# Kernel tuning notes

Measured on AMD Instinct MI355X. Metric: run time of the kernel, lower is better.

## Reference

```python
import jax, jax.numpy as jnp
import numpy as np

WS = (2, 6, 12)          # window (Wz, Wh, Ww)
SHIFT = (1, 3, 6)        # Wz//2, Wh//2, Ww//2
NUM_HEADS = 8
DIM = 256
HIDDEN = 1024            # mlp_ratio * dim
TYPE_OF_WINDOWS = 64     # (Z//Wz)*(H//Wh)
EPS = 1e-5


def _build_position_index(ws):
    Wz, Wh, Ww = ws
    zi = np.arange(Wz); zj = -np.arange(Wz) * Wz
    hi = np.arange(Wh); hj = -np.arange(Wh) * Wh
    w = np.arange(Ww)
    gzi, ghi, gw = np.meshgrid(zi, hi, w, indexing='ij')
    gzj, ghj, _ = np.meshgrid(zj, hj, w, indexing='ij')
    fi = np.stack([gzi.ravel(), ghi.ravel(), gw.ravel()])
    fj = np.stack([gzj.ravel(), ghj.ravel(), gw.ravel()])
    coords = fi[:, :, None] - fj[:, None, :]
    coords[2] += Ww - 1
    coords[1] *= 2 * Ww - 1
    coords[0] *= (2 * Ww - 1) * Wh * Wh
    return coords.sum(0).reshape(-1)  # (N*N,) int


def _window_partition(x, ws):
    # (B, Z, H, W, C) -> (B*n_windows, Wz*Wh*Ww, C)
    B, Z, H, W, C = x.shape
    Wz, Wh, Ww = ws
    x = x.reshape(B, Z // Wz, Wz, H // Wh, Wh, W // Ww, Ww, C)
    x = x.transpose(0, 1, 3, 5, 2, 4, 6, 7)
    return x.reshape(-1, Wz * Wh * Ww, C)


def _window_reverse(win, ws, B, Z, H, W):
    Wz, Wh, Ww = ws
    x = win.reshape(B, Z // Wz, H // Wh, W // Ww, Wz, Wh, Ww, -1)
    x = x.transpose(0, 1, 4, 2, 5, 3, 6, 7)
    return x.reshape(B, Z, H, W, -1)


def _build_shift_mask(Z, H, W, ws, shift):
    Wz, Wh, Ww = ws
    sz, sh, sw = shift
    img = np.zeros((1, Z, H, W, 1), dtype=np.float32)
    z_slices = (slice(0, -Wz), slice(-Wz, -sz), slice(-sz, None))
    h_slices = (slice(0, -Wh), slice(-Wh, -sh), slice(-sh, None))
    w_slices = (slice(0, -Ww), slice(-Ww, -sw), slice(-sw, None))
    cnt = 0
    for zs in z_slices:
        for hs in h_slices:
            for wsl in w_slices:
                img[:, zs, hs, wsl, :] = cnt
                cnt += 1
    m = _window_partition(img, ws)[..., 0]             # (n_w, N)
    am = m[:, None, :] - m[:, :, None]                 # (n_w, N, N)
    am = np.where(am != 0, -100.0, 0.0).astype(np.float32)
    return am[:, None]                                 # (n_w, 1, N, N)


def _ln(x, g, b):
    mu = x.mean(-1, keepdims=True)
    var = ((x - mu) ** 2).mean(-1, keepdims=True)
    return (x - mu) * jax.lax.rsqrt(var + EPS) * g + b


def setup_inputs() -> dict:
    key = jax.random.key(0)
    ks = jax.random.split(key, 16)
    B, Z, H, W, C = 1, 8, 96, 192, DIM
    n_unique = (2 * WS[2] - 1) * WS[1] * WS[1] * WS[0] * WS[0]  # 3312
    s = 0.02
    return {
        'x': jax.random.normal(ks[0], (B, Z * H * W, C), jnp.float32),
        'g1': jnp.ones((C,), jnp.float32),
        'beta1': jnp.zeros((C,), jnp.float32),
        'wqkv': jax.random.normal(ks[1], (3 * C, C), jnp.float32) * s,
        'bqkv': jnp.zeros((3 * C,), jnp.float32),
        'bias_table': jax.random.normal(ks[2], (n_unique, TYPE_OF_WINDOWS, NUM_HEADS), jnp.float32) * s,
        'wproj': jax.random.normal(ks[3], (C, C), jnp.float32) * s,
        'bproj': jnp.zeros((C,), jnp.float32),
        'g2': jnp.ones((C,), jnp.float32),
        'beta2': jnp.zeros((C,), jnp.float32),
        'w1': jax.random.normal(ks[4], (HIDDEN, C), jnp.float32) * s,
        'b1': jnp.zeros((HIDDEN,), jnp.float32),
        'w2': jax.random.normal(ks[5], (C, HIDDEN), jnp.float32) * s,
        'b2': jnp.zeros((C,), jnp.float32),
        'Z': Z, 'H': H, 'W': W, 'window_type_index': 0,
    }


def reference(x, g1, beta1, wqkv, bqkv, bias_table, wproj, bproj, g2, beta2,
              w1, b1, w2, b2, Z, H, W, window_type_index):
    B, L, C = x.shape
    hd = C // NUM_HEADS
    scale = hd ** (-0.5)
    N = WS[0] * WS[1] * WS[2]

    xs = _ln(x, g1, beta1).reshape(B, Z, H, W, C)
    # shift
    xs = jnp.roll(xs, (-SHIFT[0], -SHIFT[1], -SHIFT[2]), axis=(1, 2, 3))
    mask = jnp.asarray(_build_shift_mask(Z, H, W, WS, SHIFT))  # (n_w,1,N,N)

    win = _window_partition(xs, WS)                    # (Bw, N, C)
    Bw = win.shape[0]
    qkv = (win @ wqkv.T + bqkv).reshape(Bw, N, 3, NUM_HEADS, hd).transpose(2, 0, 3, 1, 4)
    q, k, v = qkv[0], qkv[1], qkv[2]                   # (Bw, h, N, hd)

    attn = jnp.einsum('bhnd,bhmd->bhnm', q * scale, k)
    pos_index = _build_position_index(WS)              # (N*N,)
    bias = bias_table[pos_index, window_type_index]    # (N*N, heads)
    bias = bias.reshape(N, N, NUM_HEADS).transpose(2, 0, 1)[None]
    attn = attn + bias

    n_w = mask.shape[0]
    attn = attn.reshape(B, n_w, NUM_HEADS, N, N) + mask[None]
    attn = jax.nn.softmax(attn, axis=-1).reshape(Bw, NUM_HEADS, N, N)

    out = jnp.einsum('bhnm,bhmd->bhnd', attn, v).transpose(0, 2, 1, 3).reshape(Bw, N, C)
    out = out @ wproj.T + bproj

    xr = _window_reverse(out, WS, B, Z, H, W)
    xr = jnp.roll(xr, SHIFT, axis=(1, 2, 3)).reshape(B, Z * H * W, C)

    x = x + xr
    h = _ln(x, g2, beta2)
    h = jax.nn.gelu(h @ w1.T + b1, approximate=False)
    h = h @ w2.T + b2
    return x + h
```

## Files before the change

### kernel.cpp

```cpp
#include <hip/hip_runtime.h>
#include <hip/hip_bf16.h>
#include <math.h>

#define L_TOK   147456
#define CDIM    256
#define C3      768
#define HID     1024
#define NWIN    1024
#define NTOK    144
#define NHEADS  8
#define HD      32
#define SCALE   0.1767766952966369f

typedef __attribute__((ext_vector_type(8))) short bfrag;
typedef __attribute__((ext_vector_type(4))) float f32x4;

__device__ __forceinline__ ushort f2bf(float f) {
    __hip_bfloat16 h = __float2bfloat16(f);
    return *reinterpret_cast<ushort*>(&h);
}
__device__ __forceinline__ float bf2f(ushort u) {
    __hip_bfloat16 h = *reinterpret_cast<__hip_bfloat16*>(&u);
    return __bfloat162float(h);
}

__device__ __forceinline__ void gld16(const ushort* g, ushort* l) {
    __builtin_amdgcn_global_load_lds(
        (const __attribute__((address_space(1))) void*)g,
        (__attribute__((address_space(3))) void*)l, 16, 0, 0);
}

__device__ __forceinline__ int shift_src(int gt) {
    const int win = gt / NTOK;
    const int nt  = gt - win * NTOK;
    const int wz = win >> 8, wh = (win >> 4) & 15, ww = win & 15;
    const int lz = nt / 72;
    const int t2 = nt - lz * 72;
    const int lh = t2 / 12, lw = t2 - lh * 12;
    const int z = (wz * 2 + lz + 1) & 7;
    int h = wh * 6 + lh + 3;  if (h >= 96)  h -= 96;
    int w = ww * 12 + lw + 6; if (w >= 192) w -= 192;
    return (z * 96 + h) * 192 + w;
}

__global__ __launch_bounds__(256) void ln1_kernel(const float* __restrict__ x,
                                                  const float* __restrict__ g,
                                                  const float* __restrict__ b,
                                                  ushort* __restrict__ xw,
                                                  int row0)
{
    const int wave = threadIdx.x >> 6;
    const int lane = threadIdx.x & 63;
    const int t = blockIdx.x * 4 + wave;
    const int src = shift_src(row0 + t);
    const float4 xv = *(const float4*)(x + (size_t)src * CDIM + lane * 4);
    float s  = xv.x + xv.y + xv.z + xv.w;
    float ss = xv.x*xv.x + xv.y*xv.y + xv.z*xv.z + xv.w*xv.w;
    #pragma unroll
    for (int off = 32; off; off >>= 1) {
        s  += __shfl_xor(s,  off);
        ss += __shfl_xor(ss, off);
    }
    const float mean = s * (1.0f / CDIM);
    const float var  = ss * (1.0f / CDIM) - mean * mean;
    const float rstd = rsqrtf(var + 1e-5f);
    const float4 gv = *(const float4*)(g + lane * 4);
    const float4 bv = *(const float4*)(b + lane * 4);
    union { ushort u[4]; uint2 q; } pk;
    pk.u[0] = f2bf((xv.x - mean) * rstd * gv.x + bv.x);
    pk.u[1] = f2bf((xv.y - mean) * rstd * gv.y + bv.y);
    pk.u[2] = f2bf((xv.z - mean) * rstd * gv.z + bv.z);
    pk.u[3] = f2bf((xv.w - mean) * rstd * gv.w + bv.w);
    *(uint2*)(xw + (size_t)t * CDIM + lane * 4) = pk.q;
}

__global__ __launch_bounds__(256) void cvt_kernel(const float* __restrict__ s,
                                                  ushort* __restrict__ d)
{
    const int i = (blockIdx.x * 256 + threadIdx.x) * 4;
    const float4 v = *(const float4*)(s + i);
    d[i + 0] = f2bf(v.x); d[i + 1] = f2bf(v.y);
    d[i + 2] = f2bf(v.z); d[i + 3] = f2bf(v.w);
}

__global__ __launch_bounds__(256) void comb_pre_kernel(const float* __restrict__ bt,
                                                       const int* __restrict__ wti_p,
                                                       float* __restrict__ comb)
{
    const int e = blockIdx.x * 256 + threadIdx.x;
    const int wti = *wti_p;
    const int reg  = e & 3;
    const int lane = (e >> 2) & 63;
    const int t    = e >> 8;
    const int ct = t % 9;
    const int rb = (t / 9) % 9;
    const int h  = (t / 81) % 8;
    const int cls = t / 648;
    const int i = rb * 16 + ((lane >> 4) << 2) + reg;
    const int j = ct * 16 + (lane & 15);
    const int zi = i / 72, ri = i - zi * 72, hi = ri / 12, wi = ri - (ri / 12) * 12;
    const int zj = j / 72, rj = j - zj * 72, hj = rj / 12, wj = rj - (rj / 12) * 12;
    const int idx = (zi + 2 * zj) * 828 + (hi + 6 * hj) * 23 + (wi - wj + 11);
    const float bias = bt[((size_t)idx * 64 + wti) * 8 + h];
    const int cz = (cls >> 2) & 1, ch = (cls >> 1) & 1, cw = cls & 1;
    const int ri_ = (cz ? (zi == 0 ? 1 : 2) : 0) * 9
                  + (ch ? (hi < 3 ? 1 : 2) : 0) * 3
                  + (cw ? (wi < 6 ? 1 : 2) : 0);
    const int rj_ = (cz ? (zj == 0 ? 1 : 2) : 0) * 9
                  + (ch ? (hj < 3 ? 1 : 2) : 0) * 3
                  + (cw ? (wj < 6 ? 1 : 2) : 0);
    comb[e] = bias + ((ri_ == rj_) ? 0.0f : -100.0f);
}

__global__ __launch_bounds__(64) void attn_kernel(const ushort* __restrict__ qkv,
                                                  const float* __restrict__ comb,
                                                  ushort* __restrict__ outb,
                                                  int win0)
{
    __shared__ ushort vt[32][168];
    __shared__ ushort pt[16][168];

    const int winl = blockIdx.x >> 3;
    const int head = blockIdx.x & 7;
    const int win  = win0 + winl;
    const int lane = threadIdx.x;
    const int g = lane >> 4, c = lane & 15;
    const int cls = (((win >> 8) == 3) ? 4 : 0)
                  | ((((win >> 4) & 15) == 15) ? 2 : 0)
                  | (((win & 15) == 15) ? 1 : 0);

    const ushort* qb = qkv + (((size_t)(winl * 3 + 0) * 8 + head) * NTOK) * HD;
    const ushort* kb = qkv + (((size_t)(winl * 3 + 1) * 8 + head) * NTOK) * HD;
    const ushort* vb = qkv + (((size_t)(winl * 3 + 2) * 8 + head) * NTOK) * HD;

    for (int i = lane; i < 512; i += 64) vt[i >> 4][144 + (i & 15)] = 0;
    for (int i = lane; i < 256; i += 64) pt[i >> 4][144 + (i & 15)] = 0;
    for (int base = lane * 8; base < NTOK * HD; base += 512) {
        const int j = base >> 5, d0 = base & 31;
        union { ushort u[8]; uint4 q; } tv;
        tv.q = *(const uint4*)(vb + base);
        #pragma unroll
        for (int e = 0; e < 8; ++e) vt[d0 + e][j] = tv.u[e];
    }
    __syncthreads();

    bfrag kf[9];
    #pragma unroll
    for (int ct = 0; ct < 9; ++ct)
        kf[ct] = *(const bfrag*)(kb + (size_t)(ct * 16 + c) * HD + g * 8);
    bfrag vf[2][5];
    #pragma unroll
    for (int nt = 0; nt < 2; ++nt)
        #pragma unroll
        for (int kt = 0; kt < 5; ++kt)
            vf[nt][kt] = *(const bfrag*)&vt[nt * 16 + c][kt * 32 + g * 8];

    const float* cb = comb + ((size_t)cls * 8 + head) * 81 * 256;

    for (int rb = 0; rb < 9; ++rb) {
        const bfrag aq = *(const bfrag*)(qb + (size_t)(rb * 16 + c) * HD + g * 8);
        f32x4 s[9];
        #pragma unroll
        for (int ct = 0; ct < 9; ++ct)
            s[ct] = __builtin_amdgcn_mfma_f32_16x16x32_bf16(
                aq, kf[ct], (f32x4){0.0f, 0.0f, 0.0f, 0.0f}, 0, 0, 0);

        #pragma unroll
        for (int ct = 0; ct < 9; ++ct) {
            const float4 bw = *(const float4*)(cb + (size_t)(rb * 9 + ct) * 256 + lane * 4);
            s[ct][0] = s[ct][0] * SCALE + bw.x;
            s[ct][1] = s[ct][1] * SCALE + bw.y;
            s[ct][2] = s[ct][2] * SCALE + bw.z;
            s[ct][3] = s[ct][3] * SCALE + bw.w;
        }

        float mx[4] = {-1e30f, -1e30f, -1e30f, -1e30f};
        #pragma unroll
        for (int ct = 0; ct < 9; ++ct)
            #pragma unroll
            for (int r = 0; r < 4; ++r) mx[r] = fmaxf(mx[r], s[ct][r]);
        #pragma unroll
        for (int off = 1; off < 16; off <<= 1)
            #pragma unroll
            for (int r = 0; r < 4; ++r) mx[r] = fmaxf(mx[r], __shfl_xor(mx[r], off));
        float sm[4] = {0.0f, 0.0f, 0.0f, 0.0f};
        #pragma unroll
        for (int ct = 0; ct < 9; ++ct)
            #pragma unroll
            for (int r = 0; r < 4; ++r) {
                const float e = __expf(s[ct][r] - mx[r]);
                s[ct][r] = e; sm[r] += e;
            }
        #pragma unroll
        for (int off = 1; off < 16; off <<= 1)
            #pragma unroll
            for (int r = 0; r < 4; ++r) sm[r] += __shfl_xor(sm[r], off);
        float inv[4];
        #pragma unroll
        for (int r = 0; r < 4; ++r) inv[r] = 1.0f / sm[r];

        #pragma unroll
        for (int ct = 0; ct < 9; ++ct)
            #pragma unroll
            for (int r = 0; r < 4; ++r)
                pt[g * 4 + r][ct * 16 + c] = f2bf(s[ct][r]);

        f32x4 o[2] = {(f32x4){0,0,0,0}, (f32x4){0,0,0,0}};
        #pragma unroll
        for (int kt = 0; kt < 5; ++kt) {
            const bfrag pa = *(const bfrag*)&pt[c][kt * 32 + g * 8];
            o[0] = __builtin_amdgcn_mfma_f32_16x16x32_bf16(pa, vf[0][kt], o[0], 0, 0, 0);
            o[1] = __builtin_amdgcn_mfma_f32_16x16x32_bf16(pa, vf[1][kt], o[1], 0, 0, 0);
        }

        const size_t ob = ((size_t)winl * NTOK + rb * 16 + g * 4) * CDIM + head * HD;
        #pragma unroll
        for (int nt = 0; nt < 2; ++nt)
            #pragma unroll
            for (int r = 0; r < 4; ++r)
                outb[ob + (size_t)r * CDIM + nt * 16 + c] = f2bf(o[nt][r] * inv[r]);
    }
}

template<int EPI>
__global__ __launch_bounds__(256) void mgemm(const ushort* __restrict__ A,
                                             const ushort* __restrict__ Bw,
                                             const float* __restrict__ bias,
                                             void* __restrict__ outp,
                                             const float* __restrict__ resid,
                                             int K, int grow0)
{
    __shared__ __align__(16) ushort Asb[128 * 64];
    __shared__ __align__(16) ushort Bsb[128 * 64];

    const int tid = threadIdx.x;
    const int m0 = blockIdx.y * 128;
    const int n0 = blockIdx.x * 128;
    const int w = tid >> 6, lane = tid & 63;
    const int wm = w >> 1, wn = w & 1;
    const int fr = lane & 15, kg = lane >> 4;
    const int wbase = tid & 192;

    f32x4 acc[4][4];
    #pragma unroll
    for (int i = 0; i < 4; ++i)
        #pragma unroll
        for (int j = 0; j < 4; ++j)
            acc[i][j] = (f32x4){0.0f, 0.0f, 0.0f, 0.0f};

    int lrow[4], lsl[4];
    #pragma unroll
    for (int it = 0; it < 4; ++it) {
        const int s = it * 256 + tid;
        lrow[it] = s >> 3;
        lsl[it]  = ((s & 7) ^ (lrow[it] & 7)) * 8;
    }

    size_t aoff[4], boff[4];
    #pragma unroll
    for (int it = 0; it < 4; ++it) {
        aoff[it] = (size_t)(m0 + lrow[it]) * K;
        boff[it] = (size_t)(n0 + lrow[it]) * K;
    }

    for (int kt = 0; kt < K; kt += 64) {
        #pragma unroll
        for (int it = 0; it < 4; ++it)
            gld16(A + aoff[it] + kt + lsl[it], &Asb[(it * 256 + wbase) * 8]);
        #pragma unroll
        for (int it = 0; it < 4; ++it)
            gld16(Bw + boff[it] + kt + lsl[it], &Bsb[(it * 256 + wbase) * 8]);
        __syncthreads();

        #pragma unroll
        for (int kh = 0; kh < 2; ++kh) {
            bfrag af[4], bfv[4];
            #pragma unroll
            for (int fm = 0; fm < 4; ++fm) {
                const int r = wm * 64 + fm * 16 + fr;
                af[fm] = *(const bfrag*)&Asb[r * 64 + (((kh * 4 + kg) ^ (r & 7)) * 8)];
            }
            #pragma unroll
            for (int fn = 0; fn < 4; ++fn) {
                const int r = wn * 64 + fn * 16 + fr;
                bfv[fn] = *(const bfrag*)&Bsb[r * 64 + (((kh * 4 + kg) ^ (r & 7)) * 8)];
            }
            #pragma unroll
            for (int fm = 0; fm < 4; ++fm)
                #pragma unroll
                for (int fn = 0; fn < 4; ++fn)
                    acc[fm][fn] = __builtin_amdgcn_mfma_f32_16x16x32_bf16(
                        af[fm], bfv[fn], acc[fm][fn], 0, 0, 0);
        }
        __syncthreads();
    }

    #pragma unroll
    for (int fn = 0; fn < 4; ++fn) {
        const int col = n0 + wn * 64 + fn * 16 + fr;
        const float bv = bias[col];
        #pragma unroll
        for (int fm = 0; fm < 4; ++fm) {
            #pragma unroll
            for (int r = 0; r < 4; ++r) {
                const int mi = m0 + wm * 64 + fm * 16 + kg * 4 + r;
                float val = acc[fm][fn][r] + bv;
                if constexpr (EPI == 0) {
                    const int winl = mi / NTOK, nt = mi - (mi / NTOK) * NTOK;
                    const int sel = col >> 8, head = (col >> 5) & 7, d = col & 31;
                    ((ushort*)outp)[(((size_t)(winl * 3 + sel) * 8 + head) * NTOK + nt) * HD + d] = f2bf(val);
                } else {
                    const int p = shift_src(grow0 + mi);
                    ((float*)outp)[(size_t)p * CDIM + col] = resid[(size_t)p * CDIM + col] + val;
                }
            }
        }
    }
}

__global__ __launch_bounds__(256) void mlp_fused(float* __restrict__ io,
                                                 const ushort* __restrict__ w1b,
                                                 const float* __restrict__ b1,
                                                 const ushort* __restrict__ w2b,
                                                 const float* __restrict__ b2,
                                                 const float* __restrict__ g2,
                                                 const float* __restrict__ beta2)
{
    __shared__ __align__(16) ushort lds[20480];
    ushort* XS = lds;
    ushort* HS = lds + 8192;
    ushort* SB = lds + 12288;

    const int tid = threadIdx.x;
    const int wn = tid >> 6, lane = tid & 63;
    const int fr = lane & 15, kg = lane >> 4;
    const int wbase = tid & 192;
    const int grow0 = blockIdx.x * 32;

    {
        const int row = tid >> 3;
        const int oct = tid & 7;
        const float* xr = io + (size_t)(grow0 + row) * CDIM + oct * 32;
        float4 v[8];
        float s = 0.0f, ss = 0.0f;
        #pragma unroll
        for (int j = 0; j < 8; ++j) {
            v[j] = *(const float4*)(xr + j * 4);
            s  += v[j].x + v[j].y + v[j].z + v[j].w;
            ss += v[j].x*v[j].x + v[j].y*v[j].y + v[j].z*v[j].z + v[j].w*v[j].w;
        }
        #pragma unroll
        for (int off = 1; off < 8; off <<= 1) {
            s  += __shfl_xor(s,  off);
            ss += __shfl_xor(ss, off);
        }
        const float mean = s * (1.0f / CDIM);
        const float var  = ss * (1.0f / CDIM) - mean * mean;
        const float rstd = rsqrtf(var + 1e-5f);
        #pragma unroll
        for (int j = 0; j < 4; ++j) {
            const int c = oct * 32 + j * 8;
            const float4 ga = *(const float4*)(g2 + c);
            const float4 gb = *(const float4*)(g2 + c + 4);
            const float4 ba = *(const float4*)(beta2 + c);
            const float4 bb = *(const float4*)(beta2 + c + 4);
            union { ushort u[8]; uint4 q4; } pk;
            pk.u[0] = f2bf((v[2*j].x   - mean) * rstd * ga.x + ba.x);
            pk.u[1] = f2bf((v[2*j].y   - mean) * rstd * ga.y + ba.y);
            pk.u[2] = f2bf((v[2*j].z   - mean) * rstd * ga.z + ba.z);
            pk.u[3] = f2bf((v[2*j].w   - mean) * rstd * ga.w + ba.w);
            pk.u[4] = f2bf((v[2*j+1].x - mean) * rstd * gb.x + bb.x);
            pk.u[5] = f2bf((v[2*j+1].y - mean) * rstd * gb.y + bb.y);
            pk.u[6] = f2bf((v[2*j+1].z - mean) * rstd * gb.z + bb.z);
            pk.u[7] = f2bf((v[2*j+1].w - mean) * rstd * gb.w + bb.w);
            const int slot = oct * 4 + j;
            *(uint4*)&XS[row * 256 + (slot ^ (row & 7)) * 8] = pk.q4;
        }
    }

    f32x4 acc[2][4];
    #pragma unroll
    for (int i = 0; i < 2; ++i)
        #pragma unroll
        for (int j = 0; j < 4; ++j)
            acc[i][j] = (f32x4){0.0f, 0.0f, 0.0f, 0.0f};

    for (int s = 0; s < 8; ++s) {
        f32x4 c1[2][2];
        #pragma unroll
        for (int i = 0; i < 2; ++i) { c1[i][0] = (f32x4){0,0,0,0}; c1[i][1] = (f32x4){0,0,0,0}; }
        for (int kt = 0; kt < 4; ++kt) {
            __syncthreads();
            #pragma unroll
            for (int i = 0; i < 4; ++i) {
                const int L = i * 256 + tid;
                const int row = L >> 3;
                const int sl = (L & 7) ^ (row & 7);
                gld16(w1b + (size_t)(s * 128 + row) * 256 + kt * 64 + sl * 8,
                      &SB[(i * 256 + wbase) * 8]);
            }
            __syncthreads();
            #pragma unroll
            for (int ks = 0; ks < 2; ++ks) {
                bfrag af[2], bw[2];
                #pragma unroll
                for (int fm = 0; fm < 2; ++fm) {
                    const int r = fm * 16 + fr;
                    const int slot = kt * 8 + ks * 4 + kg;
                    af[fm] = *(const bfrag*)&XS[r * 256 + (slot ^ (r & 7)) * 8];
                }
                #pragma unroll
                for (int fn = 0; fn < 2; ++fn) {
                    const int r = wn * 32 + fn * 16 + fr;
                    const int slot = ks * 4 + kg;
                    bw[fn] = *(const bfrag*)&SB[r * 64 + (slot ^ (r & 7)) * 8];
                }
                #pragma unroll
                for (int fm = 0; fm < 2; ++fm)
                    #pragma unroll
                    for (int fn = 0; fn < 2; ++fn)
                        c1[fm][fn] = __builtin_amdgcn_mfma_f32_16x16x32_bf16(
                            af[fm], bw[fn], c1[fm][fn], 0, 0, 0);
            }
        }
        #pragma unroll
        for (int fn = 0; fn < 2; ++fn) {
            const int colh = wn * 32 + fn * 16 + fr;
            const float b1v = b1[s * 128 + colh];
            #pragma unroll
            for (int fm = 0; fm < 2; ++fm) {
                #pragma unroll
                for (int r = 0; r < 4; ++r) {
                    const int mi = fm * 16 + kg * 4 + r;
                    const float v = c1[fm][fn][r] + b1v;
                    const float ge = 0.5f * v * (1.0f + erff(v * 0.70710678118654752f));
                    HS[mi * 128 + ((colh >> 3) ^ (mi & 7)) * 8 + (colh & 7)] = f2bf(ge);
                }
            }
        }
        for (int kt2 = 0; kt2 < 4; ++kt2) {
            __syncthreads();
            #pragma unroll
            for (int i = 0; i < 4; ++i) {
                const int L = i * 256 + tid;
                const int row = L >> 2;
                const int sl = (L & 3) ^ ((row >> 1) & 3);
                gld16(w2b + (size_t)row * 1024 + s * 128 + kt2 * 32 + sl * 8,
                      &SB[(i * 256 + wbase) * 8]);
            }
            __syncthreads();
            bfrag af[2], bw[4];
            #pragma unroll
            for (int fm = 0; fm < 2; ++fm) {
                const int r = fm * 16 + fr;
                af[fm] = *(const bfrag*)&HS[r * 128 + (((kt2 * 4 + kg) ^ (r & 7)) * 8)];
            }
            #pragma unroll
            for (int fn = 0; fn < 4; ++fn) {
                const int r = wn * 64 + fn * 16 + fr;
                bw[fn] = *(const bfrag*)&SB[r * 32 + ((kg ^ ((r >> 1) & 3)) * 8)];
            }
            #pragma unroll
            for (int fm = 0; fm < 2; ++fm)
                #pragma unroll
                for (int fn = 0; fn < 4; ++fn)
                    acc[fm][fn] = __builtin_amdgcn_mfma_f32_16x16x32_bf16(
                        af[fm], bw[fn], acc[fm][fn], 0, 0, 0);
        }
        __syncthreads();
    }

    #pragma unroll
    for (int fn = 0; fn < 4; ++fn) {
        const int col = wn * 64 + fn * 16 + fr;
        const float bv = b2[col];
        #pragma unroll
        for (int fm = 0; fm < 2; ++fm) {
            #pragma unroll
            for (int r = 0; r < 4; ++r) {
                const int mi = fm * 16 + kg * 4 + r;
                const size_t gi = (size_t)(grow0 + mi) * CDIM + col;
                io[gi] += acc[fm][fn][r] + bv;
            }
        }
    }
}

extern "C" void kernel_launch(void* const* d_in, const int* in_sizes, int n_in,
                              void* d_out, int out_size, void* d_ws, size_t ws_size,
                              hipStream_t stream)
{
    const float* x     = (const float*)d_in[0];
    const float* g1    = (const float*)d_in[1];
    const float* beta1 = (const float*)d_in[2];
    const float* wqkv  = (const float*)d_in[3];
    const float* bqkv  = (const float*)d_in[4];
    const float* btab  = (const float*)d_in[5];
    const float* wproj = (const float*)d_in[6];
    const float* bproj = (const float*)d_in[7];
    const float* g2    = (const float*)d_in[8];
    const float* beta2 = (const float*)d_in[9];
    const float* w1    = (const float*)d_in[10];
    const float* b1    = (const float*)d_in[11];
    const float* w2    = (const float*)d_in[12];
    const float* b2    = (const float*)d_in[13];
    const int*   wti   = (const int*)d_in[17];
    float* out = (float*)d_out;

    const size_t COMB_ELEMS = (size_t)8 * 8 * 81 * 256;
    const size_t WQKV_E = (size_t)C3 * CDIM, WP_E = (size_t)CDIM * CDIM;
    const size_t W1_E = (size_t)HID * CDIM,  W2_E = (size_t)CDIM * HID;
    const size_t base_bytes = COMB_ELEMS * 4
                            + (WQKV_E + WP_E + W1_E + W2_E) * 2;

    int nch = 32;
    for (int cand : {4, 8, 16, 32}) {
        const size_t rows = (size_t)L_TOK / cand;
        if (base_bytes + rows * (C3 + CDIM) * 2 <= ws_size) { nch = cand; break; }
    }
    const int wins_per = NWIN / nch;
    const int rows_per = wins_per * NTOK;

    char* wsp = (char*)d_ws;
    float* comb = (float*)wsp;   wsp += COMB_ELEMS * 4;
    ushort* wq_b = (ushort*)wsp; wsp += WQKV_E * 2;
    ushort* wp_b = (ushort*)wsp; wsp += WP_E * 2;
    ushort* w1_b = (ushort*)wsp; wsp += W1_E * 2;
    ushort* w2_b = (ushort*)wsp; wsp += W2_E * 2;
    ushort* ratt = (ushort*)wsp; wsp += (size_t)rows_per * CDIM * 2;
    ushort* rbig = (ushort*)wsp;

    cvt_kernel<<<(int)(WQKV_E / 1024), 256, 0, stream>>>(wqkv, wq_b);
    cvt_kernel<<<(int)(WP_E   / 1024), 256, 0, stream>>>(wproj, wp_b);
    cvt_kernel<<<(int)(W1_E   / 1024), 256, 0, stream>>>(w1, w1_b);
    cvt_kernel<<<(int)(W2_E   / 1024), 256, 0, stream>>>(w2, w2_b);
    comb_pre_kernel<<<(int)(COMB_ELEMS / 256), 256, 0, stream>>>(btab, wti, comb);

    for (int c = 0; c < nch; ++c) {
        const int row0 = c * rows_per;
        const int win0 = c * wins_per;
        ln1_kernel<<<rows_per / 4, 256, 0, stream>>>(x, g1, beta1, ratt, row0);
        mgemm<0><<<dim3(C3 / 128, rows_per / 128), 256, 0, stream>>>(
            ratt, wq_b, bqkv, rbig, nullptr, CDIM, row0);
        attn_kernel<<<wins_per * NHEADS, 64, 0, stream>>>(rbig, comb, ratt, win0);
        mgemm<1><<<dim3(CDIM / 128, rows_per / 128), 256, 0, stream>>>(
            ratt, wp_b, bproj, out, x, CDIM, row0);
    }

    mlp_fused<<<L_TOK / 32, 256, 0, stream>>>(out, w1_b, b1, w2_b, b2, g2, beta2);
}
```

Baseline: 794.7 us.

## Load MLP weight fragments directly from global memory instead of LDS staging

Drops the LDS staging buffer for the W1/W2 tiles in the fused MLP kernel. Each wave now reads its bf16 weight fragments straight from global memory (served by L2/L1), which removes most of the block barriers and shrinks LDS use so more blocks can be resident. The cost is uncoalesced 16-byte global loads whose latency is exposed right before the MFMAs, and the same weights are fetched redundantly across waves and blocks.

```diff
diff --git a/kernel.cpp b/kernel.cpp
--- a/kernel.cpp
+++ b/kernel.cpp
@@ -326,15 +326,13 @@
                                                  const float* __restrict__ g2,
                                                  const float* __restrict__ beta2)
 {
-    __shared__ __align__(16) ushort lds[20480];
+    __shared__ __align__(16) ushort lds[12288];
     ushort* XS = lds;
     ushort* HS = lds + 8192;
-    ushort* SB = lds + 12288;
 
     const int tid = threadIdx.x;
     const int wn = tid >> 6, lane = tid & 63;
     const int fr = lane & 15, kg = lane >> 4;
-    const int wbase = tid & 192;
     const int grow0 = blockIdx.x * 32;
 
     {
@@ -377,6 +375,7 @@
             *(uint4*)&XS[row * 256 + (slot ^ (row & 7)) * 8] = pk.q4;
         }
     }
+    __syncthreads();
 
     f32x4 acc[2][4];
     #pragma unroll
@@ -389,17 +388,8 @@
         f32x4 c1[2][2];
         #pragma unroll
         for (int i = 0; i < 2; ++i) { c1[i][0] = (f32x4){0,0,0,0}; c1[i][1] = (f32x4){0,0,0,0}; }
+        #pragma unroll
         for (int kt = 0; kt < 4; ++kt) {
-            __syncthreads();
-            #pragma unroll
-            for (int i = 0; i < 4; ++i) {
-                const int L = i * 256 + tid;
-                const int row = L >> 3;
-                const int sl = (L & 7) ^ (row & 7);
-                gld16(w1b + (size_t)(s * 128 + row) * 256 + kt * 64 + sl * 8,
-                      &SB[(i * 256 + wbase) * 8]);
-            }
-            __syncthreads();
             #pragma unroll
             for (int ks = 0; ks < 2; ++ks) {
                 bfrag af[2], bw[2];
@@ -411,9 +401,9 @@
                 }
                 #pragma unroll
                 for (int fn = 0; fn < 2; ++fn) {
-                    const int r = wn * 32 + fn * 16 + fr;
-                    const int slot = ks * 4 + kg;
-                    bw[fn] = *(const bfrag*)&SB[r * 64 + (slot ^ (r & 7)) * 8];
+                    const int rc = wn * 32 + fn * 16 + fr;
+                    bw[fn] = *(const bfrag*)(w1b + (size_t)(s * 128 + rc) * 256
+                                             + kt * 64 + ks * 32 + kg * 8);
                 }
                 #pragma unroll
                 for (int fm = 0; fm < 2; ++fm)
@@ -423,6 +413,9 @@
                             af[fm], bw[fn], c1[fm][fn], 0, 0, 0);
             }
         }
+
+        if (s) __syncthreads();
+
         #pragma unroll
         for (int fn = 0; fn < 2; ++fn) {
             const int colh = wn * 32 + fn * 16 + fr;
@@ -438,17 +431,10 @@
                 }
             }
         }
+        __syncthreads();
+
+        #pragma unroll
         for (int kt2 = 0; kt2 < 4; ++kt2) {
-            __syncthreads();
-            #pragma unroll
-            for (int i = 0; i < 4; ++i) {
-                const int L = i * 256 + tid;
-                const int row = L >> 2;
-                const int sl = (L & 3) ^ ((row >> 1) & 3);
-                gld16(w2b + (size_t)row * 1024 + s * 128 + kt2 * 32 + sl * 8,
-                      &SB[(i * 256 + wbase) * 8]);
-            }
-            __syncthreads();
             bfrag af[2], bw[4];
             #pragma unroll
             for (int fm = 0; fm < 2; ++fm) {
@@ -457,8 +443,9 @@
             }
             #pragma unroll
             for (int fn = 0; fn < 4; ++fn) {
-                const int r = wn * 64 + fn * 16 + fr;
-                bw[fn] = *(const bfrag*)&SB[r * 32 + ((kg ^ ((r >> 1) & 3)) * 8)];
+                const int rc = wn * 64 + fn * 16 + fr;
+                bw[fn] = *(const bfrag*)(w2b + (size_t)rc * 1024
+                                         + s * 128 + kt2 * 32 + kg * 8);
             }
             #pragma unroll
             for (int fm = 0; fm < 2; ++fm)
@@ -467,7 +454,6 @@
                     acc[fm][fn] = __builtin_amdgcn_mfma_f32_16x16x32_bf16(
                         af[fm], bw[fn], acc[fm][fn], 0, 0, 0);
         }
-        __syncthreads();
     }
 
     #pragma unroll
```

Result: slower. 1.096 ms (+37.9%).
